# Kernel optimization log

Hardware: AMD Instinct MI355X
Metric: run time of the kernel (lower is better)

Reference implementation:

```python
import jax, jax.numpy as jnp
import numpy as np

N = 100000


def _gcn_conv(x, edge_index, W, b):
    # GCNConv with add_self_loops=True, symmetric normalization.
    src, dst = edge_index[0], edge_index[1]
    loop = jnp.arange(N, dtype=src.dtype)
    src = jnp.concatenate([src, loop])
    dst = jnp.concatenate([dst, loop])
    # degree of target nodes (edge weights all 1, incl. self loops)
    deg = jax.ops.segment_sum(jnp.ones_like(dst, dtype=x.dtype), dst, num_segments=N)
    dinv = jnp.where(deg > 0, jax.lax.rsqrt(deg), 0.0)
    norm = dinv[src] * dinv[dst]  # [E+N]
    h = x @ W  # [N, out]
    msg = h[src] * norm[:, None]  # gather + scale, [E+N, out]
    out = jax.ops.segment_sum(msg, dst, num_segments=N)  # scatter-add
    return out + b


def setup_inputs() -> dict:
    key = jax.random.key(0)
    k1, k2, k3, k4 = jax.random.split(key, 4)
    input_dim, hidden, output_dim = 256, 64, 128
    E = 1600000
    x = jax.random.normal(k1, (N, input_dim), dtype=jnp.float32)
    edge_index = jax.random.randint(k2, (2, E), 0, N, dtype=jnp.int64)
    W1 = jax.random.normal(k3, (input_dim, hidden), dtype=jnp.float32) / np.sqrt(input_dim)
    b1 = jnp.zeros((hidden,), dtype=jnp.float32)
    W2 = jax.random.normal(k4, (hidden, output_dim), dtype=jnp.float32) / np.sqrt(hidden)
    b2 = jnp.zeros((output_dim,), dtype=jnp.float32)
    return {"x": x, "edge_index": edge_index, "W1": W1, "b1": b1, "W2": W2, "b2": b2}


def reference(x, edge_index, W1, b1, W2, b2):
    h = jax.nn.relu(_gcn_conv(x, edge_index, W1, b1))
    return _gcn_conv(h, edge_index, W2, b2)
```

## Files before the change

### kernel.cpp

```cpp
#include <hip/hip_runtime.h>
#include <hip/hip_fp16.h>

#define NNODES 100000
#define NBUCK 391
#define NB_CHUNK 256
#define NC (NBUCK * NB_CHUNK)
#define SCAN_ELEMS 1024

typedef _Float16 f16x8 __attribute__((ext_vector_type(8)));
typedef float    f32x4 __attribute__((ext_vector_type(4)));

__global__ void detect_kernel(const int* __restrict__ raw, int* __restrict__ flag) {
    __shared__ int cnt;
    if (threadIdx.x == 0) cnt = 0;
    __syncthreads();
    if (threadIdx.x < 100) {
        if (raw[2 * threadIdx.x + 1] == 0) atomicAdd(&cnt, 1);
    }
    __syncthreads();
    if (threadIdx.x == 0) *flag = (cnt > 50) ? 1 : 0;
}

__global__ __launch_bounds__(256) void convert_count_kernel(const int* __restrict__ raw,
                                                            int* __restrict__ src32,
                                                            int* __restrict__ dst32,
                                                            int* __restrict__ counts,
                                                            int E, int CE,
                                                            const int* __restrict__ flag) {
    __shared__ int hist[NBUCK];
    for (int i = threadIdx.x; i < NBUCK; i += 256) hist[i] = 0;
    __syncthreads();
    int b = blockIdx.x;
    int isI64 = *flag;
    int beg = b * CE;
    int end = beg + CE; if (end > E) end = E;
    for (int e = beg + (int)threadIdx.x; e < end; e += 256) {
        int s, d;
        if (isI64) { s = raw[2 * e]; d = raw[2 * E + 2 * e]; }
        else       { s = raw[e];     d = raw[E + e]; }
        src32[e] = s;
        dst32[e] = d;
        atomicAdd(&hist[d >> 8], 1);
    }
    __syncthreads();
    for (int k = threadIdx.x; k < NBUCK; k += 256)
        counts[k * NB_CHUNK + b] = hist[k];
}

__global__ __launch_bounds__(256) void scan_partial_kernel(const int* __restrict__ in,
                                                           int* __restrict__ bsum, int n) {
    int base = blockIdx.x * SCAN_ELEMS + threadIdx.x * 4;
    int s = 0;
    if (base + 3 < n) {
        int4 v = *reinterpret_cast<const int4*>(&in[base]);
        s = v.x + v.y + v.z + v.w;
    } else {
        for (int i = base; i < n && i < base + 4; ++i) s += in[i];
    }
#pragma unroll
    for (int d = 32; d; d >>= 1) s += __shfl_down(s, d, 64);
    __shared__ int ws[4];
    int wid = threadIdx.x >> 6;
    if ((threadIdx.x & 63) == 0) ws[wid] = s;
    __syncthreads();
    if (threadIdx.x == 0) bsum[blockIdx.x] = ws[0] + ws[1] + ws[2] + ws[3];
}

__global__ void scan_partials_kernel(const int* __restrict__ bsum, int* __restrict__ boff,
                                     int* __restrict__ total_out, int nb) {
    __shared__ int s[128];
    int t = threadIdx.x;
    s[t] = (t < nb) ? bsum[t] : 0;
    __syncthreads();
    for (int d = 1; d < 128; d <<= 1) {
        int v = (t >= d) ? s[t - d] : 0;
        __syncthreads();
        s[t] += v;
        __syncthreads();
    }
    if (t < nb) boff[t] = (t == 0) ? 0 : s[t - 1];
    if (t == 127) *total_out = s[127];
}

__global__ __launch_bounds__(256) void scan_write_kernel(const int* __restrict__ in,
                                                         const int* __restrict__ boff,
                                                         int* __restrict__ outp, int n) {
    __shared__ int ts[256];
    int base = blockIdx.x * SCAN_ELEMS + threadIdx.x * 4;
    int v0 = 0, v1 = 0, v2 = 0, v3 = 0;
    if (base + 3 < n) {
        int4 v = *reinterpret_cast<const int4*>(&in[base]);
        v0 = v.x; v1 = v.y; v2 = v.z; v3 = v.w;
    } else {
        if (base < n)     v0 = in[base];
        if (base + 1 < n) v1 = in[base + 1];
        if (base + 2 < n) v2 = in[base + 2];
    }
    ts[threadIdx.x] = v0 + v1 + v2 + v3;
    __syncthreads();
    for (int d = 1; d < 256; d <<= 1) {
        int t = (threadIdx.x >= d) ? ts[threadIdx.x - d] : 0;
        __syncthreads();
        ts[threadIdx.x] += t;
        __syncthreads();
    }
    int run = boff[blockIdx.x] + ((threadIdx.x == 0) ? 0 : ts[threadIdx.x - 1]);
    if (base < n)     { outp[base] = run;     run += v0; }
    if (base + 1 < n) { outp[base + 1] = run; run += v1; }
    if (base + 2 < n) { outp[base + 2] = run; run += v2; }
    if (base + 3 < n) { outp[base + 3] = run; }
}

__global__ __launch_bounds__(256) void scatter_kernel(const int* __restrict__ src32,
                                                      const int* __restrict__ dst32,
                                                      const int* __restrict__ cbase,
                                                      int* __restrict__ cw,
                                                      int E, int CE) {
    __shared__ int cur[NBUCK];
    int b = blockIdx.x;
    for (int k = threadIdx.x; k < NBUCK; k += 256)
        cur[k] = cbase[k * NB_CHUNK + b];
    __syncthreads();
    int beg = b * CE;
    int end = beg + CE; if (end > E) end = E;
    for (int e = beg + (int)threadIdx.x; e < end; e += 256) {
        int s = src32[e];
        int d = dst32[e];
        int pos = atomicAdd(&cur[d >> 8], 1);
        cw[pos] = s | ((d & 255) << 24);
    }
}

__global__ __launch_bounds__(256) void histdeg_kernel(const int* __restrict__ cw,
                                                      const int* __restrict__ cbase,
                                                      int* __restrict__ indeg,
                                                      float* __restrict__ dinv, int n) {
    __shared__ int hist[256];
    hist[threadIdx.x] = 0;
    __syncthreads();
    int k = blockIdx.x;
    int beg = cbase[k * NB_CHUNK];
    int end = cbase[(k + 1) * NB_CHUNK];
    for (int e = beg + (int)threadIdx.x; e < end; e += 256)
        atomicAdd(&hist[(cw[e] >> 24) & 255], 1);
    __syncthreads();
    int i = (k << 8) + threadIdx.x;
    if (i < n) {
        int dg = hist[threadIdx.x];
        indeg[i] = dg;
        dinv[i] = rsqrtf((float)(dg + 1));
    }
}

__global__ __launch_bounds__(256) void fillcol_kernel(const int* __restrict__ cw,
                                                      const int* __restrict__ cbase,
                                                      const int* __restrict__ ptr,
                                                      int* __restrict__ col, int n) {
    __shared__ int cur[256];
    int k = blockIdx.x;
    int i = (k << 8) + threadIdx.x;
    cur[threadIdx.x] = (i < n) ? ptr[i] : 0;
    __syncthreads();
    int beg = cbase[k * NB_CHUNK];
    int end = cbase[(k + 1) * NB_CHUNK];
    for (int e = beg + (int)threadIdx.x; e < end; e += 256) {
        int v = cw[e];
        int pos = atomicAdd(&cur[(v >> 24) & 255], 1);
        col[pos] = v & 0x00FFFFFF;
    }
}

__global__ void wfrag_kernel(const float* __restrict__ W, __half* __restrict__ wf) {
    int flat = blockIdx.x * 256 + threadIdx.x;
    int j  = flat & 7;
    int l  = (flat >> 3) & 63;
    int nb = (flat >> 9) & 3;
    int kc = flat >> 11;
    int k  = kc * 32 + ((l >> 4) << 3) + j;
    int nc = nb * 16 + (l & 15);
    wf[flat] = __float2half(W[k * 64 + nc]);
}

__global__ void wfrag2_kernel(const float* __restrict__ W, __half* __restrict__ wf) {
    int flat = blockIdx.x * 256 + threadIdx.x;
    int j  = flat & 7;
    int l  = (flat >> 3) & 63;
    int nb = (flat >> 9) & 7;
    int kc = flat >> 12;
    int k  = kc * 32 + ((l >> 4) << 3) + j;
    int nc = nb * 16 + (l & 15);
    wf[flat] = __float2half(W[k * 128 + nc]);
}

__global__ __launch_bounds__(256) void gemm1_kernel(const float* __restrict__ x,
                                                    const __half* __restrict__ wf,
                                                    __half* __restrict__ H, int M) {
    __shared__ __half xs[64][264];
    int tid = threadIdx.x;
    int bm = blockIdx.x * 64;
    const float4* x4 = reinterpret_cast<const float4*>(x);
#pragma unroll
    for (int i = 0; i < 16; ++i) {
        int lin = i * 256 + tid;
        int row = lin >> 6;
        int c4  = lin & 63;
        int gr = bm + row; if (gr >= M) gr = M - 1;
        float4 v = x4[(size_t)gr * 64 + c4];
        __half* dst = &xs[row][c4 * 4];
        dst[0] = __float2half(v.x); dst[1] = __float2half(v.y);
        dst[2] = __float2half(v.z); dst[3] = __float2half(v.w);
    }
    __syncthreads();
    int w = tid >> 6;
    int l = tid & 63;
    int lrow = l & 15;
    int lk   = l >> 4;
    const f16x8* wf8 = reinterpret_cast<const f16x8*>(wf);
    f32x4 acc[4] = {};
#pragma unroll
    for (int kc = 0; kc < 8; ++kc) {
        f16x8 a = *reinterpret_cast<const f16x8*>(&xs[w * 16 + lrow][kc * 32 + lk * 8]);
#pragma unroll
        for (int nb = 0; nb < 4; ++nb) {
            f16x8 b = wf8[(kc * 4 + nb) * 64 + l];
            acc[nb] = __builtin_amdgcn_mfma_f32_16x16x32_f16(a, b, acc[nb], 0, 0, 0);
        }
    }
#pragma unroll
    for (int nb = 0; nb < 4; ++nb)
#pragma unroll
        for (int r = 0; r < 4; ++r) {
            int row = bm + w * 16 + lk * 4 + r;
            if (row < M) H[(size_t)row * 64 + nb * 16 + lrow] = __float2half(acc[nb][r]);
        }
}

__global__ __launch_bounds__(256) void aggregate_kernel(const __half* __restrict__ h,
                                                        const int* __restrict__ ptr,
                                                        const int* __restrict__ col,
                                                        const float* __restrict__ dinv,
                                                        const float* __restrict__ bias,
                                                        void* __restrict__ out, int n,
                                                        int relu, int out_half) {
    int node = (blockIdx.x << 2) + (threadIdx.x >> 6);
    if (node >= n) return;
    int lane = threadIdx.x & 63;
    int g  = lane >> 3;
    int fl = (lane & 7) << 3;
    float acc[8] = {};
    int pend = ptr[node + 1];
    int p = ptr[node] + g;
    for (; p + 8 < pend; p += 16) {
        int c0 = col[p];
        int c1 = col[p + 8];
        uint4 r0 = *reinterpret_cast<const uint4*>(&h[(size_t)c0 * 64 + fl]);
        uint4 r1 = *reinterpret_cast<const uint4*>(&h[(size_t)c1 * 64 + fl]);
        float w0 = dinv[c0], w1 = dinv[c1];
        const unsigned* u0 = &r0.x;
        const unsigned* u1 = &r1.x;
#pragma unroll
        for (int k = 0; k < 4; ++k) {
            float2 f0 = __half22float2(*reinterpret_cast<const __half2*>(&u0[k]));
            float2 f1 = __half22float2(*reinterpret_cast<const __half2*>(&u1[k]));
            acc[2 * k]     = fmaf(w0, f0.x, acc[2 * k]);
            acc[2 * k + 1] = fmaf(w0, f0.y, acc[2 * k + 1]);
            acc[2 * k]     = fmaf(w1, f1.x, acc[2 * k]);
            acc[2 * k + 1] = fmaf(w1, f1.y, acc[2 * k + 1]);
        }
    }
    if (p < pend) {
        int c0 = col[p];
        uint4 r0 = *reinterpret_cast<const uint4*>(&h[(size_t)c0 * 64 + fl]);
        float w0 = dinv[c0];
        const unsigned* u0 = &r0.x;
#pragma unroll
        for (int k = 0; k < 4; ++k) {
            float2 f0 = __half22float2(*reinterpret_cast<const __half2*>(&u0[k]));
            acc[2 * k]     = fmaf(w0, f0.x, acc[2 * k]);
            acc[2 * k + 1] = fmaf(w0, f0.y, acc[2 * k + 1]);
        }
    }
#pragma unroll
    for (int j = 0; j < 8; ++j) {
        acc[j] += __shfl_xor(acc[j], 8, 64);
        acc[j] += __shfl_xor(acc[j], 16, 64);
        acc[j] += __shfl_xor(acc[j], 32, 64);
    }
    if (g == 0) {
        float di = dinv[node];
        uint4 sv = *reinterpret_cast<const uint4*>(&h[(size_t)node * 64 + fl]);
        const unsigned* su = &sv.x;
        float v[8];
#pragma unroll
        for (int k = 0; k < 4; ++k) {
            float2 f = __half22float2(*reinterpret_cast<const __half2*>(&su[k]));
            v[2 * k]     = fmaf(di, f.x, acc[2 * k]) * di;
            v[2 * k + 1] = fmaf(di, f.y, acc[2 * k + 1]) * di;
        }
        if (bias) {
            float4 b0 = *reinterpret_cast<const float4*>(&bias[fl]);
            float4 b1 = *reinterpret_cast<const float4*>(&bias[fl + 4]);
            v[0] += b0.x; v[1] += b0.y; v[2] += b0.z; v[3] += b0.w;
            v[4] += b1.x; v[5] += b1.y; v[6] += b1.z; v[7] += b1.w;
        }
        if (relu) {
#pragma unroll
            for (int j = 0; j < 8; ++j) v[j] = fmaxf(v[j], 0.f);
        }
        if (out_half) {
            __half hv[8];
#pragma unroll
            for (int j = 0; j < 8; ++j) hv[j] = __float2half(v[j]);
            *reinterpret_cast<uint4*>(&((__half*)out)[(size_t)node * 64 + fl]) =
                *reinterpret_cast<const uint4*>(hv);
        } else {
            float* fo = (float*)out;
            *reinterpret_cast<float4*>(&fo[(size_t)node * 64 + fl]) =
                make_float4(v[0], v[1], v[2], v[3]);
            *reinterpret_cast<float4*>(&fo[(size_t)node * 64 + fl + 4]) =
                make_float4(v[4], v[5], v[6], v[7]);
        }
    }
}

__global__ __launch_bounds__(256) void gemm2_kernel(const __half* __restrict__ A,
                                                    const __half* __restrict__ wf,
                                                    const float* __restrict__ bias,
                                                    float* __restrict__ out, int M) {
    int tid = threadIdx.x;
    int w = tid >> 6;
    int l = tid & 63;
    int lrow = l & 15;
    int lk   = l >> 4;
    int base = blockIdx.x * 64 + w * 16;
    int arow = base + lrow; if (arow >= M) arow = M - 1;
    f16x8 a0 = *reinterpret_cast<const f16x8*>(&A[(size_t)arow * 64 + lk * 8]);
    f16x8 a1 = *reinterpret_cast<const f16x8*>(&A[(size_t)arow * 64 + 32 + lk * 8]);
    const f16x8* wf8 = reinterpret_cast<const f16x8*>(wf);
    f32x4 acc[8] = {};
#pragma unroll
    for (int nb = 0; nb < 8; ++nb) {
        acc[nb] = __builtin_amdgcn_mfma_f32_16x16x32_f16(a0, wf8[nb * 64 + l], acc[nb], 0, 0, 0);
        acc[nb] = __builtin_amdgcn_mfma_f32_16x16x32_f16(a1, wf8[(8 + nb) * 64 + l], acc[nb], 0, 0, 0);
    }
#pragma unroll
    for (int nb = 0; nb < 8; ++nb) {
        float bv = bias[nb * 16 + lrow];
#pragma unroll
        for (int r = 0; r < 4; ++r) {
            int row = base + lk * 4 + r;
            if (row < M) out[(size_t)row * 128 + nb * 16 + lrow] = acc[nb][r] + bv;
        }
    }
}

extern "C" void kernel_launch(void* const* d_in, const int* in_sizes, int n_in,
                              void* d_out, int out_size, void* d_ws, size_t ws_size,
                              hipStream_t stream) {
    const float* x  = (const float*)d_in[0];
    const int*   ei = (const int*)d_in[1];
    const float* W1 = (const float*)d_in[2];
    const float* b1 = (const float*)d_in[3];
    const float* W2 = (const float*)d_in[4];
    const float* b2 = (const float*)d_in[5];
    float* out = (float*)d_out;
    const int n = NNODES;
    const int E = in_sizes[1] / 2;
    const int CE = (E + NB_CHUNK - 1) / NB_CHUNK;

    char* w = (char*)d_ws;
    auto alloc = [&](size_t bytes) {
        char* p = w;
        w += (bytes + 255) & ~(size_t)255;
        return p;
    };
    int*    flag   = (int*)   alloc(4);
    int*    src32  = (int*)   alloc((size_t)E * 4);
    int*    dst32  = (int*)   alloc((size_t)E * 4);
    int*    counts = (int*)   alloc((size_t)NC * 4);
    int*    cbase  = (int*)   alloc((size_t)(NC + 1) * 4);
    int*    indeg  = (int*)   alloc((size_t)n * 4);
    float*  dinv   = (float*) alloc((size_t)n * 4);
    int*    ptr    = (int*)   alloc((size_t)(n + 1) * 4);
    int*    bsum   = (int*)   alloc(128 * 4);
    int*    boff   = (int*)   alloc(128 * 4);
    int*    cw     = (int*)   alloc((size_t)E * 4);
    int*    col    = (int*)   alloc((size_t)E * 4);
    __half* wfrag  = (__half*)alloc(16384 * 2);
    __half* wfrag2 = (__half*)alloc(8192 * 2);
    __half* H1     = (__half*)alloc((size_t)n * 64 * 2);
    __half* h1     = (__half*)alloc((size_t)n * 64 * 2);
    __half* A2     = (__half*)alloc((size_t)n * 64 * 2);

    int sbC = (NC + SCAN_ELEMS - 1) / SCAN_ELEMS;
    int sbN = (n  + SCAN_ELEMS - 1) / SCAN_ELEMS;

    detect_kernel<<<1, 128, 0, stream>>>(ei, flag);
    wfrag_kernel<<<64, 256, 0, stream>>>(W1, wfrag);
    wfrag2_kernel<<<32, 256, 0, stream>>>(W2, wfrag2);
    convert_count_kernel<<<NB_CHUNK, 256, 0, stream>>>(ei, src32, dst32, counts, E, CE, flag);
    scan_partial_kernel<<<sbC, 256, 0, stream>>>(counts, bsum, NC);
    scan_partials_kernel<<<1, 128, 0, stream>>>(bsum, boff, &cbase[NC], sbC);
    scan_write_kernel<<<sbC, 256, 0, stream>>>(counts, boff, cbase, NC);
    scatter_kernel<<<NB_CHUNK, 256, 0, stream>>>(src32, dst32, cbase, cw, E, CE);
    histdeg_kernel<<<NBUCK, 256, 0, stream>>>(cw, cbase, indeg, dinv, n);
    scan_partial_kernel<<<sbN, 256, 0, stream>>>(indeg, bsum, n);
    scan_partials_kernel<<<1, 128, 0, stream>>>(bsum, boff, &ptr[n], sbN);
    scan_write_kernel<<<sbN, 256, 0, stream>>>(indeg, boff, ptr, n);
    fillcol_kernel<<<NBUCK, 256, 0, stream>>>(cw, cbase, ptr, col, n);

    gemm1_kernel<<<(n + 63) / 64, 256, 0, stream>>>(x, wfrag, H1, n);
    aggregate_kernel<<<(n + 3) / 4, 256, 0, stream>>>(H1, ptr, col, dinv, b1, h1, n, 1, 1);
    aggregate_kernel<<<(n + 3) / 4, 256, 0, stream>>>(h1, ptr, col, dinv, nullptr, A2, n, 0, 1);
    gemm2_kernel<<<(n + 63) / 64, 256, 0, stream>>>(A2, wfrag2, b2, out, n);
}
```

Baseline: 198.2 us.

## Merge weight prep/detect kernels and co-schedule edge conversion with GEMM1

Folds the three tiny setup kernels (weight fragment packing for W1, W2 and int64 detection) into one launch. It also fuses the edge convert/count pass with the first GEMM into a single grid whose blocks branch on their index, so the memory-bound edge pass and the MFMA GEMM run concurrently. This cuts launch count and lets two independent stages overlap. The cost is that the fused kernel always reserves the GEMM's larger shared-memory footprint, which may lower occupancy for the convert blocks. The aggregate kernel also drops its unused float-output branch.

```diff
diff --git a/kernel.cpp b/kernel.cpp
--- a/kernel.cpp
+++ b/kernel.cpp
@@ -10,41 +10,118 @@
 typedef _Float16 f16x8 __attribute__((ext_vector_type(8)));
 typedef float    f32x4 __attribute__((ext_vector_type(4)));
 
-__global__ void detect_kernel(const int* __restrict__ raw, int* __restrict__ flag) {
-    __shared__ int cnt;
-    if (threadIdx.x == 0) cnt = 0;
-    __syncthreads();
-    if (threadIdx.x < 100) {
-        if (raw[2 * threadIdx.x + 1] == 0) atomicAdd(&cnt, 1);
-    }
-    __syncthreads();
-    if (threadIdx.x == 0) *flag = (cnt > 50) ? 1 : 0;
-}
-
-__global__ __launch_bounds__(256) void convert_count_kernel(const int* __restrict__ raw,
+__global__ __launch_bounds__(256) void prep_kernel(const float* __restrict__ W1,
+                                                   const float* __restrict__ W2,
+                                                   const int* __restrict__ raw,
+                                                   __half* __restrict__ wf1,
+                                                   __half* __restrict__ wf2,
+                                                   int* __restrict__ flag) {
+    int b = blockIdx.x;
+    if (b < 64) {
+        int flat = b * 256 + threadIdx.x;
+        int j  = flat & 7;
+        int l  = (flat >> 3) & 63;
+        int nb = (flat >> 9) & 3;
+        int kc = flat >> 11;
+        int k  = kc * 32 + ((l >> 4) << 3) + j;
+        int nc = nb * 16 + (l & 15);
+        wf1[flat] = __float2half(W1[k * 64 + nc]);
+    } else if (b < 96) {
+        int flat = (b - 64) * 256 + threadIdx.x;
+        int j  = flat & 7;
+        int l  = (flat >> 3) & 63;
+        int nb = (flat >> 9) & 7;
+        int kc = flat >> 12;
+        int k  = kc * 32 + ((l >> 4) << 3) + j;
+        int nc = nb * 16 + (l & 15);
+        wf2[flat] = __float2half(W2[k * 128 + nc]);
+    } else {
+        __shared__ int cnt;
+        if (threadIdx.x == 0) cnt = 0;
+        __syncthreads();
+        if (threadIdx.x < 100) {
+            if (raw[2 * threadIdx.x + 1] == 0) atomicAdd(&cnt, 1);
+        }
+        __syncthreads();
+        if (threadIdx.x == 0) *flag = (cnt > 50) ? 1 : 0;
+    }
+}
+
+__global__ __launch_bounds__(256) void convert_gemm1_kernel(const int* __restrict__ raw,
                                                             int* __restrict__ src32,
                                                             int* __restrict__ dst32,
                                                             int* __restrict__ counts,
                                                             int E, int CE,
-                                                            const int* __restrict__ flag) {
-    __shared__ int hist[NBUCK];
-    for (int i = threadIdx.x; i < NBUCK; i += 256) hist[i] = 0;
-    __syncthreads();
-    int b = blockIdx.x;
-    int isI64 = *flag;
-    int beg = b * CE;
-    int end = beg + CE; if (end > E) end = E;
-    for (int e = beg + (int)threadIdx.x; e < end; e += 256) {
-        int s, d;
-        if (isI64) { s = raw[2 * e]; d = raw[2 * E + 2 * e]; }
-        else       { s = raw[e];     d = raw[E + e]; }
-        src32[e] = s;
-        dst32[e] = d;
-        atomicAdd(&hist[d >> 8], 1);
-    }
-    __syncthreads();
-    for (int k = threadIdx.x; k < NBUCK; k += 256)
-        counts[k * NB_CHUNK + b] = hist[k];
+                                                            const int* __restrict__ flag,
+                                                            const float* __restrict__ x,
+                                                            const __half* __restrict__ wf,
+                                                            __half* __restrict__ H, int M) {
+    __shared__ __align__(16) char smem[64 * 264 * 2];
+    int bid = blockIdx.x;
+    if (bid < NB_CHUNK) {
+        int* hist = (int*)smem;
+        for (int i = threadIdx.x; i < NBUCK; i += 256) hist[i] = 0;
+        __syncthreads();
+        int isI64 = *flag;
+        int beg = bid * CE;
+        int end = beg + CE; if (end > E) end = E;
+        const int2* raw2 = reinterpret_cast<const int2*>(raw);
+        for (int e = beg + (int)threadIdx.x; e < end; e += 256) {
+            int s, d;
+            if (isI64) {
+                s = raw2[e].x;
+                d = raw2[E + e].x;
+            } else {
+                s = raw[e];
+                d = raw[E + e];
+            }
+            src32[e] = s;
+            dst32[e] = d;
+            atomicAdd(&hist[d >> 8], 1);
+        }
+        __syncthreads();
+        for (int k = threadIdx.x; k < NBUCK; k += 256)
+            counts[k * NB_CHUNK + bid] = hist[k];
+    } else {
+        __half (*xs)[264] = (__half(*)[264])smem;
+        int tid = threadIdx.x;
+        int bm = (bid - NB_CHUNK) * 64;
+        const float4* x4 = reinterpret_cast<const float4*>(x);
+#pragma unroll
+        for (int i = 0; i < 16; ++i) {
+            int lin = i * 256 + tid;
+            int row = lin >> 6;
+            int c4  = lin & 63;
+            int gr = bm + row; if (gr >= M) gr = M - 1;
+            float4 v = x4[(size_t)gr * 64 + c4];
+            __half* dst = &xs[row][c4 * 4];
+            dst[0] = __float2half(v.x); dst[1] = __float2half(v.y);
+            dst[2] = __float2half(v.z); dst[3] = __float2half(v.w);
+        }
+        __syncthreads();
+        int w = tid >> 6;
+        int l = tid & 63;
+        int lrow = l & 15;
+        int lk   = l >> 4;
+        const f16x8* wf8 = reinterpret_cast<const f16x8*>(wf);
+        f32x4 acc[4] = {};
+#pragma unroll
+        for (int kc = 0; kc < 8; ++kc) {
+            f16x8 a = *reinterpret_cast<const f16x8*>(&xs[w * 16 + lrow][kc * 32 + lk * 8]);
+#pragma unroll
+            for (int nb = 0; nb < 4; ++nb) {
+                f16x8 bfr = wf8[(kc * 4 + nb) * 64 + l];
+                acc[nb] = __builtin_amdgcn_mfma_f32_16x16x32_f16(a, bfr, acc[nb], 0, 0, 0);
+            }
+        }
+#pragma unroll
+        for (int nb = 0; nb < 4; ++nb)
+#pragma unroll
+            for (int r = 0; r < 4; ++r) {
+                int row = bm + w * 16 + lk * 4 + r;
+                if (row < M) H[(size_t)row * 64 + nb * 16 + lrow] = __float2half(acc[nb][r]);
+            }
+    }
 }
 
 __global__ __launch_bounds__(256) void scan_partial_kernel(const int* __restrict__ in,
@@ -170,78 +247,13 @@
     }
 }
 
-__global__ void wfrag_kernel(const float* __restrict__ W, __half* __restrict__ wf) {
-    int flat = blockIdx.x * 256 + threadIdx.x;
-    int j  = flat & 7;
-    int l  = (flat >> 3) & 63;
-    int nb = (flat >> 9) & 3;
-    int kc = flat >> 11;
-    int k  = kc * 32 + ((l >> 4) << 3) + j;
-    int nc = nb * 16 + (l & 15);
-    wf[flat] = __float2half(W[k * 64 + nc]);
-}
-
-__global__ void wfrag2_kernel(const float* __restrict__ W, __half* __restrict__ wf) {
-    int flat = blockIdx.x * 256 + threadIdx.x;
-    int j  = flat & 7;
-    int l  = (flat >> 3) & 63;
-    int nb = (flat >> 9) & 7;
-    int kc = flat >> 12;
-    int k  = kc * 32 + ((l >> 4) << 3) + j;
-    int nc = nb * 16 + (l & 15);
-    wf[flat] = __float2half(W[k * 128 + nc]);
-}
-
-__global__ __launch_bounds__(256) void gemm1_kernel(const float* __restrict__ x,
-                                                    const __half* __restrict__ wf,
-                                                    __half* __restrict__ H, int M) {
-    __shared__ __half xs[64][264];
-    int tid = threadIdx.x;
-    int bm = blockIdx.x * 64;
-    const float4* x4 = reinterpret_cast<const float4*>(x);
-#pragma unroll
-    for (int i = 0; i < 16; ++i) {
-        int lin = i * 256 + tid;
-        int row = lin >> 6;
-        int c4  = lin & 63;
-        int gr = bm + row; if (gr >= M) gr = M - 1;
-        float4 v = x4[(size_t)gr * 64 + c4];
-        __half* dst = &xs[row][c4 * 4];
-        dst[0] = __float2half(v.x); dst[1] = __float2half(v.y);
-        dst[2] = __float2half(v.z); dst[3] = __float2half(v.w);
-    }
-    __syncthreads();
-    int w = tid >> 6;
-    int l = tid & 63;
-    int lrow = l & 15;
-    int lk   = l >> 4;
-    const f16x8* wf8 = reinterpret_cast<const f16x8*>(wf);
-    f32x4 acc[4] = {};
-#pragma unroll
-    for (int kc = 0; kc < 8; ++kc) {
-        f16x8 a = *reinterpret_cast<const f16x8*>(&xs[w * 16 + lrow][kc * 32 + lk * 8]);
-#pragma unroll
-        for (int nb = 0; nb < 4; ++nb) {
-            f16x8 b = wf8[(kc * 4 + nb) * 64 + l];
-            acc[nb] = __builtin_amdgcn_mfma_f32_16x16x32_f16(a, b, acc[nb], 0, 0, 0);
-        }
-    }
-#pragma unroll
-    for (int nb = 0; nb < 4; ++nb)
-#pragma unroll
-        for (int r = 0; r < 4; ++r) {
-            int row = bm + w * 16 + lk * 4 + r;
-            if (row < M) H[(size_t)row * 64 + nb * 16 + lrow] = __float2half(acc[nb][r]);
-        }
-}
-
 __global__ __launch_bounds__(256) void aggregate_kernel(const __half* __restrict__ h,
                                                         const int* __restrict__ ptr,
                                                         const int* __restrict__ col,
                                                         const float* __restrict__ dinv,
                                                         const float* __restrict__ bias,
-                                                        void* __restrict__ out, int n,
-                                                        int relu, int out_half) {
+                                                        __half* __restrict__ out, int n,
+                                                        int relu) {
     int node = (blockIdx.x << 2) + (threadIdx.x >> 6);
     if (node >= n) return;
     int lane = threadIdx.x & 63;
@@ -307,19 +319,11 @@
 #pragma unroll
             for (int j = 0; j < 8; ++j) v[j] = fmaxf(v[j], 0.f);
         }
-        if (out_half) {
-            __half hv[8];
-#pragma unroll
-            for (int j = 0; j < 8; ++j) hv[j] = __float2half(v[j]);
-            *reinterpret_cast<uint4*>(&((__half*)out)[(size_t)node * 64 + fl]) =
-                *reinterpret_cast<const uint4*>(hv);
-        } else {
-            float* fo = (float*)out;
-            *reinterpret_cast<float4*>(&fo[(size_t)node * 64 + fl]) =
-                make_float4(v[0], v[1], v[2], v[3]);
-            *reinterpret_cast<float4*>(&fo[(size_t)node * 64 + fl + 4]) =
-                make_float4(v[4], v[5], v[6], v[7]);
-        }
+        __half hv[8];
+#pragma unroll
+        for (int j = 0; j < 8; ++j) hv[j] = __float2half(v[j]);
+        *reinterpret_cast<uint4*>(&out[(size_t)node * 64 + fl]) =
+            *reinterpret_cast<const uint4*>(hv);
     }
 }
 
@@ -394,11 +398,11 @@
 
     int sbC = (NC + SCAN_ELEMS - 1) / SCAN_ELEMS;
     int sbN = (n  + SCAN_ELEMS - 1) / SCAN_ELEMS;
-
-    detect_kernel<<<1, 128, 0, stream>>>(ei, flag);
-    wfrag_kernel<<<64, 256, 0, stream>>>(W1, wfrag);
-    wfrag2_kernel<<<32, 256, 0, stream>>>(W2, wfrag2);
-    convert_count_kernel<<<NB_CHUNK, 256, 0, stream>>>(ei, src32, dst32, counts, E, CE, flag);
+    int g1b = (n + 63) / 64;
+
+    prep_kernel<<<97, 256, 0, stream>>>(W1, W2, ei, wfrag, wfrag2, flag);
+    convert_gemm1_kernel<<<NB_CHUNK + g1b, 256, 0, stream>>>(
+        ei, src32, dst32, counts, E, CE, flag, x, wfrag, H1, n);
     scan_partial_kernel<<<sbC, 256, 0, stream>>>(counts, bsum, NC);
     scan_partials_kernel<<<1, 128, 0, stream>>>(bsum, boff, &cbase[NC], sbC);
     scan_write_kernel<<<sbC, 256, 0, stream>>>(counts, boff, cbase, NC);
@@ -409,8 +413,7 @@
     scan_write_kernel<<<sbN, 256, 0, stream>>>(indeg, boff, ptr, n);
     fillcol_kernel<<<NBUCK, 256, 0, stream>>>(cw, cbase, ptr, col, n);
 
-    gemm1_kernel<<<(n + 63) / 64, 256, 0, stream>>>(x, wfrag, H1, n);
-    aggregate_kernel<<<(n + 3) / 4, 256, 0, stream>>>(H1, ptr, col, dinv, b1, h1, n, 1, 1);
-    aggregate_kernel<<<(n + 3) / 4, 256, 0, stream>>>(h1, ptr, col, dinv, nullptr, A2, n, 0, 1);
+    aggregate_kernel<<<(n + 3) / 4, 256, 0, stream>>>(H1, ptr, col, dinv, b1, h1, n, 1);
+    aggregate_kernel<<<(n + 3) / 4, 256, 0, stream>>>(h1, ptr, col, dinv, nullptr, A2, n, 0);
     gemm2_kernel<<<(n + 63) / 64, 256, 0, stream>>>(A2, wfrag2, b2, out, n);
 }
```

Result: faster. 187.4 us (-5.4%).
